# Performance work log

Hardware: AMD Instinct MI355X
Metric: run time of the kernel (lower is better)

Reference implementation:

```python
import jax, jax.numpy as jnp
import numpy as np

EPS = 1e-5  # torch F.layer_norm default

def _layer_norm(x):
    mu = jnp.mean(x, axis=-1, keepdims=True)
    var = jnp.mean((x - mu) ** 2, axis=-1, keepdims=True)
    return (x - mu) * jax.lax.rsqrt(var + EPS)

def setup_inputs() -> dict:
    key = jax.random.key(0)
    k1, k2, k3, k4 = jax.random.split(key, 4)
    B, T, d, n = 4, 32, 256, 1024
    return {
        "x_seq": jax.random.normal(k1, (B, T, d), jnp.float32),
        "targets": jax.random.normal(k2, (B, T, d), jnp.float32),
        "E": jax.random.normal(k3, (d, n), jnp.float32) * 0.1,
        "Dy": jax.random.normal(k4, (n, d), jnp.float32) * 0.1,
    }

def reference(x_seq, targets, E, Dy):
    B, T, d = x_seq.shape
    n = E.shape[1]
    # Precompute per-step neuron activations (no cross-step dependency here)
    x_neurons = jax.nn.relu(_layer_norm(x_seq @ E))      # [B,T,n]
    tgt_neurons = jax.nn.relu(_layer_norm(targets @ E))  # [B,T,n]
    # update at step t uses targets[:, t+1]; last step does no update
    tgt_next = jnp.concatenate(
        [tgt_neurons[:, 1:], jnp.zeros_like(tgt_neurons[:, :1])], axis=1)
    upd_mask = jnp.arange(T) < (T - 1)  # [T]

    G0 = jnp.tile(0.01 * jnp.eye(n, dtype=x_seq.dtype)[None], (B, 1, 1))

    def step(G, inp):
        xn, tn, m = inp  # [B,n], [B,n], scalar bool
        p1 = jnp.einsum('bn,bnm->bm', xn, G)
        p2 = jnp.einsum('bn,bnm->bm', p1, G)
        p3 = jnp.einsum('bn,bnm->bm', p2, G)
        reasoning = jnp.maximum(p1, jnp.maximum(p2, p3))
        y = jax.nn.relu(reasoning @ Dy)  # [B,d]
        # rank-1 Hebbian max-update: G = max(G, 0.5 * xn tn^T)
        upd = 0.5 * xn[:, :, None] * tn[:, None, :]
        G_new = jnp.where(m, jnp.maximum(G, upd), G)
        return G_new, y

    xs = (jnp.swapaxes(x_neurons, 0, 1),  # [T,B,n]
          jnp.swapaxes(tgt_next, 0, 1),   # [T,B,n]
          upd_mask)                       # [T]
    _, ys = jax.lax.scan(step, G0, xs)    # ys: [T,B,d]
    return jnp.swapaxes(ys, 0, 1)         # [B,T,d]
```

## Files before the change

### kernel.cpp

```cpp
#include <hip/hip_runtime.h>

#define BB 4
#define TT 32
#define DD 256
#define NN 1024

#define XN_OFF   0
#define TN_OFF   131072
#define PB_OFF   262144
#define RB_OFF   524288
#define FLG_OFF  655360
#define FLG_WORDS 6144
#define WS_END   (FLG_OFF + FLG_WORDS)

__global__ __launch_bounds__(256) void precompute_kernel(
    const float* __restrict__ x_seq, const float* __restrict__ targets,
    const float* __restrict__ E, float* __restrict__ ws)
{
    __shared__ float xr[4][DD];
    __shared__ float redS[4][4], redSS[4][4];
    const int blk = blockIdx.x;
    const int bt0 = blk * 2, bt1 = bt0 + 1;
    const int tid = threadIdx.x;
    const int lane = tid & 63, w = tid >> 6;

    xr[0][tid] = x_seq[(size_t)bt0 * DD + tid];
    xr[1][tid] = x_seq[(size_t)bt1 * DD + tid];
    xr[2][tid] = targets[(size_t)bt0 * DD + tid];
    xr[3][tid] = targets[(size_t)bt1 * DD + tid];
    __syncthreads();

    const float4* E4 = (const float4*)E;
    float4 acc[4];
#pragma unroll
    for (int r = 0; r < 4; ++r) acc[r] = make_float4(0.f, 0.f, 0.f, 0.f);
#pragma unroll 4
    for (int k = 0; k < DD; ++k) {
        float4 e = E4[(size_t)k * (NN / 4) + tid];
#pragma unroll
        for (int r = 0; r < 4; ++r) {
            float xv = xr[r][k];
            acc[r].x += xv * e.x; acc[r].y += xv * e.y;
            acc[r].z += xv * e.z; acc[r].w += xv * e.w;
        }
    }
    float s[4], ss[4];
#pragma unroll
    for (int r = 0; r < 4; ++r) {
        s[r]  = acc[r].x + acc[r].y + acc[r].z + acc[r].w;
        ss[r] = acc[r].x*acc[r].x + acc[r].y*acc[r].y + acc[r].z*acc[r].z + acc[r].w*acc[r].w;
    }
#pragma unroll
    for (int d = 1; d < 64; d <<= 1) {
#pragma unroll
        for (int r = 0; r < 4; ++r) {
            s[r]  += __shfl_xor(s[r], d, 64);
            ss[r] += __shfl_xor(ss[r], d, 64);
        }
    }
    if (lane == 0) {
#pragma unroll
        for (int r = 0; r < 4; ++r) { redS[w][r] = s[r]; redSS[w][r] = ss[r]; }
    }
    __syncthreads();
#pragma unroll
    for (int r = 0; r < 4; ++r) {
        s[r]  = redS[0][r] + redS[1][r] + redS[2][r] + redS[3][r];
        ss[r] = redSS[0][r] + redSS[1][r] + redSS[2][r] + redSS[3][r];
    }
#pragma unroll
    for (int r = 0; r < 4; ++r) {
        const float mu  = s[r] * (1.0f / NN);
        const float var = ss[r] * (1.0f / NN) - mu * mu;
        const float inv = rsqrtf(var + 1e-5f);
        float4 o;
        o.x = fmaxf(0.f, (acc[r].x - mu) * inv);
        o.y = fmaxf(0.f, (acc[r].y - mu) * inv);
        o.z = fmaxf(0.f, (acc[r].z - mu) * inv);
        o.w = fmaxf(0.f, (acc[r].w - mu) * inv);
        const int bt = (r & 1) ? bt1 : bt0;
        float* dst = nullptr;
        if (r < 2) dst = ws + XN_OFF + (size_t)bt * NN;
        else if ((bt & 31) > 0) dst = ws + TN_OFF + (size_t)(bt - 1) * NN;
        if (dst) ((float4*)dst)[tid] = o;
    }
}

__device__ __forceinline__ float ald(const float* p) {
    return __hip_atomic_load(p, __ATOMIC_RELAXED, __HIP_MEMORY_SCOPE_AGENT);
}
__device__ __forceinline__ unsigned long long ald64(const unsigned long long* p) {
    return __hip_atomic_load(p, __ATOMIC_RELAXED, __HIP_MEMORY_SCOPE_AGENT);
}
__device__ __forceinline__ void ast(float* p, float v) {
    __hip_atomic_store(p, v, __ATOMIC_RELAXED, __HIP_MEMORY_SCOPE_AGENT);
}
__device__ __forceinline__ unsigned aldu_rlx(const unsigned* p) {
    return __hip_atomic_load(p, __ATOMIC_RELAXED, __HIP_MEMORY_SCOPE_AGENT);
}

__global__ __launch_bounds__(512, 2) void mega_kernel(
    const float* __restrict__ Dy, float* __restrict__ out, float* __restrict__ ws)
{
    __shared__ float sh[6144];
    const int blk = blockIdx.x;
    const int tid = threadIdx.x;

    float* pb     = ws + PB_OFF;
    float* rb     = ws + RB_OFF;
    unsigned* flg = (unsigned*)(ws + FLG_OFF);

    if (blk < 192) {
        const int stage = blk >> 6;
        const int b     = (blk >> 4) & 3;
        const int wg    = blk & 15;
        const int lane  = tid & 63;
        const int w     = tid >> 6;
        const int colbase = wg * 64 + w * 8;
        const int row0    = lane * 16;
        const float* xn = ws + XN_OFF + (size_t)b * TT * NN;
        const float* tn = ws + TN_OFF + (size_t)b * TT * NN;
        unsigned* myflag = flg + ((size_t)(stage * 4 + b) * 16 + wg) * 32;
        const unsigned* inflags =
            (stage > 0) ? flg + ((size_t)((stage - 1) * 4 + b) * 16) * 32 : (const unsigned*)0;
        unsigned seen = 0;

        float G[16][8];
#pragma unroll
        for (int i = 0; i < 16; ++i)
#pragma unroll
            for (int c = 0; c < 8; ++c)
                G[i][c] = (row0 + i == colbase + c) ? 0.01f : 0.0f;

#pragma unroll 1
        for (int t = 0; t < TT; ++t) {
            const int bt = b * TT + t;
            float* p1 = pb + (size_t)bt * 2 * NN;
            float* p2 = p1 + NN;

            float in[16], x[16];
            float v1own = 0.f;
            if (stage == 0) {
                const float4* xp = (const float4*)(xn + (size_t)t * NN + row0);
                float4 q0 = xp[0], q1 = xp[1], q2 = xp[2], q3 = xp[3];
                in[0]=q0.x; in[1]=q0.y; in[2]=q0.z; in[3]=q0.w;
                in[4]=q1.x; in[5]=q1.y; in[6]=q1.z; in[7]=q1.w;
                in[8]=q2.x; in[9]=q2.y; in[10]=q2.z; in[11]=q2.w;
                in[12]=q3.x; in[13]=q3.y; in[14]=q3.z; in[15]=q3.w;
#pragma unroll
                for (int j = 0; j < 16; ++j) x[j] = in[j];
            } else {
                const unsigned tgt = (unsigned)(t + 1);
                if (tid < 64) {
                    if (seen < tgt) {
                        const unsigned* p = inflags + (size_t)(tid & 15) * 32;
                        int g = 0;
                        for (;;) {
                            unsigned v = aldu_rlx(p);
                            if (v > seen) seen = v;
                            if (__all(seen >= tgt)) break;
                            __builtin_amdgcn_s_sleep(1);
                            if (++g > (1 << 22)) break;
                        }
                    }
                }
                __syncthreads();
                asm volatile("" ::: "memory");
                if (stage == 2) v1own = ald(p1 + colbase + (lane & 7));
                const float* src = (stage == 1) ? p1 : p2;
                union { unsigned long long u; float f[2]; } cv;
                cv.u = ald64((const unsigned long long*)src + tid);
                const int e0 = 2 * tid;
                sh[e0 + (e0 >> 4)]     = cv.f[0];
                sh[e0 + 1 + (e0 >> 4)] = cv.f[1];
                __syncthreads();
#pragma unroll
                for (int j = 0; j < 16; ++j) in[j] = sh[lane * 17 + j];
            }

            float acc[8] = {0.f,0.f,0.f,0.f,0.f,0.f,0.f,0.f};
#pragma unroll
            for (int i = 0; i < 16; ++i)
#pragma unroll
                for (int c = 0; c < 8; ++c) acc[c] += in[i] * G[i][c];

            float t4[8];
#pragma unroll
            for (int c = 0; c < 8; ++c) t4[c] = __shfl_xor(acc[c], 4, 64);
            const bool k2 = (lane & 4) != 0;
            float s4[4];
#pragma unroll
            for (int k = 0; k < 4; ++k) s4[k] = k2 ? (acc[4+k] + t4[4+k]) : (acc[k] + t4[k]);
            float t2[4];
#pragma unroll
            for (int k = 0; k < 4; ++k) t2[k] = __shfl_xor(s4[k], 2, 64);
            const bool k1 = (lane & 2) != 0;
            float s2[2];
#pragma unroll
            for (int k = 0; k < 2; ++k) s2[k] = k1 ? (s4[2+k] + t2[2+k]) : (s4[k] + t2[k]);
            float t1[2];
#pragma unroll
            for (int k = 0; k < 2; ++k) t1[k] = __shfl_xor(s2[k], 1, 64);
            float v = (lane & 1) ? (s2[1] + t1[1]) : (s2[0] + t1[0]);
            v += __shfl_xor(v, 8, 64);
            v += __shfl_xor(v, 16, 64);
            v += __shfl_xor(v, 32, 64);

            if (stage == 0) {
                if (lane < 8) ast(p1 + colbase + lane, v);
            } else if (stage == 1) {
                if (lane < 8) ast(p2 + colbase + lane, v);
            } else {
                const int c = colbase + (lane & 7);
                const float v2own = sh[c + (c >> 4)];
                float r = fmaxf(v, fmaxf(v1own, v2own));
                if (lane < 8) ast(rb + (size_t)bt * NN + colbase + lane, r);
            }
            __syncthreads();
            if (tid == 0)
                __hip_atomic_store(myflag, (unsigned)(t + 1),
                                   __ATOMIC_RELEASE, __HIP_MEMORY_SCOPE_AGENT);

            if (t < TT - 1) {
                if (stage != 0) {
                    const float4* xp = (const float4*)(xn + (size_t)t * NN + row0);
                    float4 q0 = xp[0], q1 = xp[1], q2 = xp[2], q3 = xp[3];
                    x[0]=q0.x; x[1]=q0.y; x[2]=q0.z; x[3]=q0.w;
                    x[4]=q1.x; x[5]=q1.y; x[6]=q1.z; x[7]=q1.w;
                    x[8]=q2.x; x[9]=q2.y; x[10]=q2.z; x[11]=q2.w;
                    x[12]=q3.x; x[13]=q3.y; x[14]=q3.z; x[15]=q3.w;
                }
                const float4 ta = *(const float4*)(tn + (size_t)t * NN + colbase);
                const float4 tb = *(const float4*)(tn + (size_t)t * NN + colbase + 4);
                const float tv[8] = {0.5f*ta.x, 0.5f*ta.y, 0.5f*ta.z, 0.5f*ta.w,
                                     0.5f*tb.x, 0.5f*tb.y, 0.5f*tb.z, 0.5f*tb.w};
#pragma unroll
                for (int c = 0; c < 8; ++c)
#pragma unroll
                    for (int i = 0; i < 16; ++i)
                        G[i][c] = fmaxf(G[i][c], x[i] * tv[c]);
            }
        }
    } else {
        const int k   = blk - 192;
        const int b   = k >> 3;
        const int t0  = (k & 7) * 4;
        const int bt0 = b * TT + t0;
        if (tid < 64) {
            const unsigned* p = flg + ((size_t)(2 * 4 + b) * 16 + (tid & 15)) * 32;
            const unsigned tgt = (unsigned)(t0 + 4);
            int g = 0;
            for (;;) {
                unsigned v = aldu_rlx(p);
                if (__all(v >= tgt)) break;
                __builtin_amdgcn_s_sleep(1);
                if (++g > (1 << 22)) break;
            }
        }
        __syncthreads();
        asm volatile("" ::: "memory");
#pragma unroll
        for (int j = 0; j < 4; ++j) {
            const float* r = rb + (size_t)(bt0 + j) * NN;
            sh[tid * 4 + j]         = ald(r + tid);
            sh[(tid + 512) * 4 + j] = ald(r + tid + 512);
        }
        __syncthreads();
        const int d = tid & 255, h = tid >> 8;
        float acc[4] = {0.f, 0.f, 0.f, 0.f};
        const int n0 = h * 512;
#pragma unroll 8
        for (int n = n0; n < n0 + 512; ++n) {
            const float dv = Dy[(size_t)n * DD + d];
            const float4 rv = *(const float4*)&sh[n * 4];
            acc[0] += rv.x * dv; acc[1] += rv.y * dv;
            acc[2] += rv.z * dv; acc[3] += rv.w * dv;
        }
#pragma unroll
        for (int j = 0; j < 4; ++j) sh[4096 + (h * 4 + j) * 256 + d] = acc[j];
        __syncthreads();
        if (tid < 256) {
#pragma unroll
            for (int j = 0; j < 4; ++j)
                out[(size_t)(bt0 + j) * DD + tid] =
                    fmaxf(0.f, sh[4096 + j * 256 + tid] + sh[4096 + (4 + j) * 256 + tid]);
        }
    }
}

extern "C" void kernel_launch(void* const* d_in, const int* in_sizes, int n_in,
                              void* d_out, int out_size, void* d_ws, size_t ws_size,
                              hipStream_t stream) {
    const float* x_seq   = (const float*)d_in[0];
    const float* targets = (const float*)d_in[1];
    const float* E       = (const float*)d_in[2];
    const float* Dy      = (const float*)d_in[3];
    float* out = (float*)d_out;
    float* ws  = (float*)d_ws;

    hipMemsetAsync(ws + FLG_OFF, 0, (size_t)FLG_WORDS * sizeof(unsigned), stream);

    precompute_kernel<<<BB * TT / 2, 256, 0, stream>>>(x_seq, targets, E, ws);
    mega_kernel<<<224, 512, 0, stream>>>(Dy, out, ws);
}
```

Baseline: 242.2 us.

## Process two timesteps per flag handshake in pipelined stage blocks

Each stage block now handles timesteps t and t+1 per loop iteration. It waits on the upstream flag once for both, loads both input vectors together, and publishes a single flag after both products. This halves the number of cross-block spin-wait handshakes and barriers, but it makes downstream stages wait for two steps before they start, so pipeline fill latency grows. Launch bounds drop to one block per SM to allow more registers for the doubled state.

```diff
diff --git a/kernel.cpp b/kernel.cpp
--- a/kernel.cpp
+++ b/kernel.cpp
@@ -99,7 +99,7 @@
     return __hip_atomic_load(p, __ATOMIC_RELAXED, __HIP_MEMORY_SCOPE_AGENT);
 }
 
-__global__ __launch_bounds__(512, 2) void mega_kernel(
+__global__ __launch_bounds__(512, 1) void mega_kernel(
     const float* __restrict__ Dy, float* __restrict__ out, float* __restrict__ ws)
 {
     __shared__ float sh[6144];
@@ -133,24 +133,31 @@
                 G[i][c] = (row0 + i == colbase + c) ? 0.01f : 0.0f;
 
 #pragma unroll 1
-        for (int t = 0; t < TT; ++t) {
+        for (int t = 0; t < TT; t += 2) {
             const int bt = b * TT + t;
-            float* p1 = pb + (size_t)bt * 2 * NN;
-            float* p2 = p1 + NN;
-
-            float in[16], x[16];
-            float v1own = 0.f;
+            float* p1t = pb + (size_t)bt * 2 * NN;
+            float* p2t = p1t + NN;
+            float* p1u = p2t + NN;
+            float* p2u = p1u + NN;
+
+            float in_t[16], in_u[16];
+            float v1own_t = 0.f, v1own_u = 0.f;
+
             if (stage == 0) {
                 const float4* xp = (const float4*)(xn + (size_t)t * NN + row0);
+                const float4* xq = (const float4*)(xn + (size_t)(t + 1) * NN + row0);
                 float4 q0 = xp[0], q1 = xp[1], q2 = xp[2], q3 = xp[3];
-                in[0]=q0.x; in[1]=q0.y; in[2]=q0.z; in[3]=q0.w;
-                in[4]=q1.x; in[5]=q1.y; in[6]=q1.z; in[7]=q1.w;
-                in[8]=q2.x; in[9]=q2.y; in[10]=q2.z; in[11]=q2.w;
-                in[12]=q3.x; in[13]=q3.y; in[14]=q3.z; in[15]=q3.w;
-#pragma unroll
-                for (int j = 0; j < 16; ++j) x[j] = in[j];
+                float4 r0 = xq[0], r1 = xq[1], r2 = xq[2], r3 = xq[3];
+                in_t[0]=q0.x; in_t[1]=q0.y; in_t[2]=q0.z; in_t[3]=q0.w;
+                in_t[4]=q1.x; in_t[5]=q1.y; in_t[6]=q1.z; in_t[7]=q1.w;
+                in_t[8]=q2.x; in_t[9]=q2.y; in_t[10]=q2.z; in_t[11]=q2.w;
+                in_t[12]=q3.x; in_t[13]=q3.y; in_t[14]=q3.z; in_t[15]=q3.w;
+                in_u[0]=r0.x; in_u[1]=r0.y; in_u[2]=r0.z; in_u[3]=r0.w;
+                in_u[4]=r1.x; in_u[5]=r1.y; in_u[6]=r1.z; in_u[7]=r1.w;
+                in_u[8]=r2.x; in_u[9]=r2.y; in_u[10]=r2.z; in_u[11]=r2.w;
+                in_u[12]=r3.x; in_u[13]=r3.y; in_u[14]=r3.z; in_u[15]=r3.w;
             } else {
-                const unsigned tgt = (unsigned)(t + 1);
+                const unsigned tgt = (unsigned)(t + 2);
                 if (tid < 64) {
                     if (seen < tgt) {
                         const unsigned* p = inflags + (size_t)(tid & 15) * 32;
@@ -166,63 +173,74 @@
                 }
                 __syncthreads();
                 asm volatile("" ::: "memory");
-                if (stage == 2) v1own = ald(p1 + colbase + (lane & 7));
-                const float* src = (stage == 1) ? p1 : p2;
-                union { unsigned long long u; float f[2]; } cv;
-                cv.u = ald64((const unsigned long long*)src + tid);
+                if (stage == 2) {
+                    v1own_t = ald(p1t + colbase + (lane & 7));
+                    v1own_u = ald(p1u + colbase + (lane & 7));
+                }
+                const float* st = (stage == 1) ? p1t : p2t;
+                const float* su = (stage == 1) ? p1u : p2u;
+                union { unsigned long long u; float f[2]; } ct, cu;
+                ct.u = ald64((const unsigned long long*)st + tid);
+                cu.u = ald64((const unsigned long long*)su + tid);
                 const int e0 = 2 * tid;
-                sh[e0 + (e0 >> 4)]     = cv.f[0];
-                sh[e0 + 1 + (e0 >> 4)] = cv.f[1];
+                sh[e0 + (e0 >> 4)]            = ct.f[0];
+                sh[e0 + 1 + (e0 >> 4)]        = ct.f[1];
+                sh[1152 + e0 + (e0 >> 4)]     = cu.f[0];
+                sh[1152 + e0 + 1 + (e0 >> 4)] = cu.f[1];
                 __syncthreads();
 #pragma unroll
-                for (int j = 0; j < 16; ++j) in[j] = sh[lane * 17 + j];
-            }
-
-            float acc[8] = {0.f,0.f,0.f,0.f,0.f,0.f,0.f,0.f};
-#pragma unroll
-            for (int i = 0; i < 16; ++i)
-#pragma unroll
-                for (int c = 0; c < 8; ++c) acc[c] += in[i] * G[i][c];
-
-            float t4[8];
-#pragma unroll
-            for (int c = 0; c < 8; ++c) t4[c] = __shfl_xor(acc[c], 4, 64);
-            const bool k2 = (lane & 4) != 0;
-            float s4[4];
-#pragma unroll
-            for (int k = 0; k < 4; ++k) s4[k] = k2 ? (acc[4+k] + t4[4+k]) : (acc[k] + t4[k]);
-            float t2[4];
-#pragma unroll
-            for (int k = 0; k < 4; ++k) t2[k] = __shfl_xor(s4[k], 2, 64);
-            const bool k1 = (lane & 2) != 0;
-            float s2[2];
-#pragma unroll
-            for (int k = 0; k < 2; ++k) s2[k] = k1 ? (s4[2+k] + t2[2+k]) : (s4[k] + t2[k]);
-            float t1[2];
-#pragma unroll
-            for (int k = 0; k < 2; ++k) t1[k] = __shfl_xor(s2[k], 1, 64);
-            float v = (lane & 1) ? (s2[1] + t1[1]) : (s2[0] + t1[0]);
-            v += __shfl_xor(v, 8, 64);
-            v += __shfl_xor(v, 16, 64);
-            v += __shfl_xor(v, 32, 64);
-
-            if (stage == 0) {
-                if (lane < 8) ast(p1 + colbase + lane, v);
-            } else if (stage == 1) {
-                if (lane < 8) ast(p2 + colbase + lane, v);
-            } else {
-                const int c = colbase + (lane & 7);
-                const float v2own = sh[c + (c >> 4)];
-                float r = fmaxf(v, fmaxf(v1own, v2own));
-                if (lane < 8) ast(rb + (size_t)bt * NN + colbase + lane, r);
-            }
-            __syncthreads();
-            if (tid == 0)
-                __hip_atomic_store(myflag, (unsigned)(t + 1),
-                                   __ATOMIC_RELEASE, __HIP_MEMORY_SCOPE_AGENT);
-
-            if (t < TT - 1) {
-                if (stage != 0) {
+                for (int j = 0; j < 16; ++j) {
+                    in_t[j] = sh[lane * 17 + j];
+                    in_u[j] = sh[1152 + lane * 17 + j];
+                }
+            }
+
+            {
+                float acc[8] = {0.f,0.f,0.f,0.f,0.f,0.f,0.f,0.f};
+#pragma unroll
+                for (int i = 0; i < 16; ++i)
+#pragma unroll
+                    for (int c = 0; c < 8; ++c) acc[c] += in_t[i] * G[i][c];
+                float t4[8];
+#pragma unroll
+                for (int c = 0; c < 8; ++c) t4[c] = __shfl_xor(acc[c], 4, 64);
+                const bool k2 = (lane & 4) != 0;
+                float s4[4];
+#pragma unroll
+                for (int k = 0; k < 4; ++k) s4[k] = k2 ? (acc[4+k] + t4[4+k]) : (acc[k] + t4[k]);
+                float t2[4];
+#pragma unroll
+                for (int k = 0; k < 4; ++k) t2[k] = __shfl_xor(s4[k], 2, 64);
+                const bool k1 = (lane & 2) != 0;
+                float s2[2];
+#pragma unroll
+                for (int k = 0; k < 2; ++k) s2[k] = k1 ? (s4[2+k] + t2[2+k]) : (s4[k] + t2[k]);
+                float t1[2];
+#pragma unroll
+                for (int k = 0; k < 2; ++k) t1[k] = __shfl_xor(s2[k], 1, 64);
+                float v = (lane & 1) ? (s2[1] + t1[1]) : (s2[0] + t1[0]);
+                v += __shfl_xor(v, 8, 64);
+                v += __shfl_xor(v, 16, 64);
+                v += __shfl_xor(v, 32, 64);
+
+                if (stage == 0) {
+                    if (lane < 8) ast(p1t + colbase + lane, v);
+                } else if (stage == 1) {
+                    if (lane < 8) ast(p2t + colbase + lane, v);
+                } else {
+                    const int c = colbase + (lane & 7);
+                    const float v2own = sh[c + (c >> 4)];
+                    float r = fmaxf(v, fmaxf(v1own_t, v2own));
+                    if (lane < 8) ast(rb + (size_t)bt * NN + colbase + lane, r);
+                }
+            }
+
+            {
+                float x[16];
+                if (stage == 0) {
+#pragma unroll
+                    for (int j = 0; j < 16; ++j) x[j] = in_t[j];
+                } else {
                     const float4* xp = (const float4*)(xn + (size_t)t * NN + row0);
                     float4 q0 = xp[0], q1 = xp[1], q2 = xp[2], q3 = xp[3];
                     x[0]=q0.x; x[1]=q0.y; x[2]=q0.z; x[3]=q0.w;
@@ -232,6 +250,75 @@
                 }
                 const float4 ta = *(const float4*)(tn + (size_t)t * NN + colbase);
                 const float4 tb = *(const float4*)(tn + (size_t)t * NN + colbase + 4);
+                const float tv[8] = {0.5f*ta.x, 0.5f*ta.y, 0.5f*ta.z, 0.5f*ta.w,
+                                     0.5f*tb.x, 0.5f*tb.y, 0.5f*tb.z, 0.5f*tb.w};
+#pragma unroll
+                for (int c = 0; c < 8; ++c)
+#pragma unroll
+                    for (int i = 0; i < 16; ++i)
+                        G[i][c] = fmaxf(G[i][c], x[i] * tv[c]);
+            }
+
+            {
+                float acc[8] = {0.f,0.f,0.f,0.f,0.f,0.f,0.f,0.f};
+#pragma unroll
+                for (int i = 0; i < 16; ++i)
+#pragma unroll
+                    for (int c = 0; c < 8; ++c) acc[c] += in_u[i] * G[i][c];
+                float t4[8];
+#pragma unroll
+                for (int c = 0; c < 8; ++c) t4[c] = __shfl_xor(acc[c], 4, 64);
+                const bool k2 = (lane & 4) != 0;
+                float s4[4];
+#pragma unroll
+                for (int k = 0; k < 4; ++k) s4[k] = k2 ? (acc[4+k] + t4[4+k]) : (acc[k] + t4[k]);
+                float t2[4];
+#pragma unroll
+                for (int k = 0; k < 4; ++k) t2[k] = __shfl_xor(s4[k], 2, 64);
+                const bool k1 = (lane & 2) != 0;
+                float s2[2];
+#pragma unroll
+                for (int k = 0; k < 2; ++k) s2[k] = k1 ? (s4[2+k] + t2[2+k]) : (s4[k] + t2[k]);
+                float t1[2];
+#pragma unroll
+                for (int k = 0; k < 2; ++k) t1[k] = __shfl_xor(s2[k], 1, 64);
+                float v = (lane & 1) ? (s2[1] + t1[1]) : (s2[0] + t1[0]);
+                v += __shfl_xor(v, 8, 64);
+                v += __shfl_xor(v, 16, 64);
+                v += __shfl_xor(v, 32, 64);
+
+                if (stage == 0) {
+                    if (lane < 8) ast(p1u + colbase + lane, v);
+                } else if (stage == 1) {
+                    if (lane < 8) ast(p2u + colbase + lane, v);
+                } else {
+                    const int c = colbase + (lane & 7);
+                    const float v2own = sh[1152 + c + (c >> 4)];
+                    float r = fmaxf(v, fmaxf(v1own_u, v2own));
+                    if (lane < 8) ast(rb + (size_t)(bt + 1) * NN + colbase + lane, r);
+                }
+            }
+
+            __syncthreads();
+            if (tid == 0)
+                __hip_atomic_store(myflag, (unsigned)(t + 2),
+                                   __ATOMIC_RELEASE, __HIP_MEMORY_SCOPE_AGENT);
+
+            if (t + 1 < TT - 1) {
+                float x[16];
+                if (stage == 0) {
+#pragma unroll
+                    for (int j = 0; j < 16; ++j) x[j] = in_u[j];
+                } else {
+                    const float4* xp = (const float4*)(xn + (size_t)(t + 1) * NN + row0);
+                    float4 q0 = xp[0], q1 = xp[1], q2 = xp[2], q3 = xp[3];
+                    x[0]=q0.x; x[1]=q0.y; x[2]=q0.z; x[3]=q0.w;
+                    x[4]=q1.x; x[5]=q1.y; x[6]=q1.z; x[7]=q1.w;
+                    x[8]=q2.x; x[9]=q2.y; x[10]=q2.z; x[11]=q2.w;
+                    x[12]=q3.x; x[13]=q3.y; x[14]=q3.z; x[15]=q3.w;
+                }
+                const float4 ta = *(const float4*)(tn + (size_t)(t + 1) * NN + colbase);
+                const float4 tb = *(const float4*)(tn + (size_t)(t + 1) * NN + colbase + 4);
                 const float tv[8] = {0.5f*ta.x, 0.5f*ta.y, 0.5f*ta.z, 0.5f*ta.w,
                                      0.5f*tb.x, 0.5f*tb.y, 0.5f*tb.z, 0.5f*tb.w};
 #pragma unroll
```

Result: faster. 213.6 us (-11.8%).

## Batch four timesteps per inter-stage flag handoff in the pipelined scan kernel

Applied to the files above, without the earlier changes.

The three-stage G-propagation pipeline now processes timesteps in chunks of four, with one flag wait and one flag publish per chunk. Previously it synchronised across blocks on every timestep. The consumer stages load four timesteps' worth of p1/p2 vectors into shared memory at once, and the Hebbian max-updates for the first three steps run inside the chunk. This is meant to cut the number of cross-block spin-wait round trips, at the cost of a coarser pipeline fill latency between stages. Launch bounds drop to one block per CU to give the compiler more registers for the unrolled chunk.

```diff
diff --git a/kernel.cpp b/kernel.cpp
--- a/kernel.cpp
+++ b/kernel.cpp
@@ -99,7 +99,7 @@
     return __hip_atomic_load(p, __ATOMIC_RELAXED, __HIP_MEMORY_SCOPE_AGENT);
 }
 
-__global__ __launch_bounds__(512, 2) void mega_kernel(
+__global__ __launch_bounds__(512, 1) void mega_kernel(
     const float* __restrict__ Dy, float* __restrict__ out, float* __restrict__ ws)
 {
     __shared__ float sh[6144];
@@ -133,24 +133,14 @@
                 G[i][c] = (row0 + i == colbase + c) ? 0.01f : 0.0f;
 
 #pragma unroll 1
-        for (int t = 0; t < TT; ++t) {
+        for (int t = 0; t < TT; t += 4) {
             const int bt = b * TT + t;
-            float* p1 = pb + (size_t)bt * 2 * NN;
-            float* p2 = p1 + NN;
-
-            float in[16], x[16];
-            float v1own = 0.f;
-            if (stage == 0) {
-                const float4* xp = (const float4*)(xn + (size_t)t * NN + row0);
-                float4 q0 = xp[0], q1 = xp[1], q2 = xp[2], q3 = xp[3];
-                in[0]=q0.x; in[1]=q0.y; in[2]=q0.z; in[3]=q0.w;
-                in[4]=q1.x; in[5]=q1.y; in[6]=q1.z; in[7]=q1.w;
-                in[8]=q2.x; in[9]=q2.y; in[10]=q2.z; in[11]=q2.w;
-                in[12]=q3.x; in[13]=q3.y; in[14]=q3.z; in[15]=q3.w;
-#pragma unroll
-                for (int j = 0; j < 16; ++j) x[j] = in[j];
-            } else {
-                const unsigned tgt = (unsigned)(t + 1);
+            float* pbase = pb + (size_t)bt * 2 * NN;
+
+            float v1own[4] = {0.f, 0.f, 0.f, 0.f};
+
+            if (stage != 0) {
+                const unsigned tgt = (unsigned)(t + 4);
                 if (tid < 64) {
                     if (seen < tgt) {
                         const unsigned* p = inflags + (size_t)(tid & 15) * 32;
@@ -166,72 +156,132 @@
                 }
                 __syncthreads();
                 asm volatile("" ::: "memory");
-                if (stage == 2) v1own = ald(p1 + colbase + (lane & 7));
-                const float* src = (stage == 1) ? p1 : p2;
-                union { unsigned long long u; float f[2]; } cv;
-                cv.u = ald64((const unsigned long long*)src + tid);
+                if (stage == 2) {
+#pragma unroll
+                    for (int j = 0; j < 4; ++j)
+                        v1own[j] = ald(pbase + (size_t)(2 * j) * NN + colbase + (lane & 7));
+                }
+                union { unsigned long long u; float f[2]; } cv[4];
+#pragma unroll
+                for (int j = 0; j < 4; ++j) {
+                    const float* src = pbase + (size_t)(2 * j) * NN + ((stage == 1) ? 0 : NN);
+                    cv[j].u = ald64((const unsigned long long*)src + tid);
+                }
                 const int e0 = 2 * tid;
-                sh[e0 + (e0 >> 4)]     = cv.f[0];
-                sh[e0 + 1 + (e0 >> 4)] = cv.f[1];
+#pragma unroll
+                for (int j = 0; j < 4; ++j) {
+                    sh[j * 1152 + e0 + (e0 >> 4)]     = cv[j].f[0];
+                    sh[j * 1152 + e0 + 1 + (e0 >> 4)] = cv[j].f[1];
+                }
                 __syncthreads();
-#pragma unroll
-                for (int j = 0; j < 16; ++j) in[j] = sh[lane * 17 + j];
             }
 
-            float acc[8] = {0.f,0.f,0.f,0.f,0.f,0.f,0.f,0.f};
-#pragma unroll
-            for (int i = 0; i < 16; ++i)
-#pragma unroll
-                for (int c = 0; c < 8; ++c) acc[c] += in[i] * G[i][c];
-
-            float t4[8];
-#pragma unroll
-            for (int c = 0; c < 8; ++c) t4[c] = __shfl_xor(acc[c], 4, 64);
-            const bool k2 = (lane & 4) != 0;
-            float s4[4];
-#pragma unroll
-            for (int k = 0; k < 4; ++k) s4[k] = k2 ? (acc[4+k] + t4[4+k]) : (acc[k] + t4[k]);
-            float t2[4];
-#pragma unroll
-            for (int k = 0; k < 4; ++k) t2[k] = __shfl_xor(s4[k], 2, 64);
-            const bool k1 = (lane & 2) != 0;
-            float s2[2];
-#pragma unroll
-            for (int k = 0; k < 2; ++k) s2[k] = k1 ? (s4[2+k] + t2[2+k]) : (s4[k] + t2[k]);
-            float t1[2];
-#pragma unroll
-            for (int k = 0; k < 2; ++k) t1[k] = __shfl_xor(s2[k], 1, 64);
-            float v = (lane & 1) ? (s2[1] + t1[1]) : (s2[0] + t1[0]);
-            v += __shfl_xor(v, 8, 64);
-            v += __shfl_xor(v, 16, 64);
-            v += __shfl_xor(v, 32, 64);
-
-            if (stage == 0) {
-                if (lane < 8) ast(p1 + colbase + lane, v);
-            } else if (stage == 1) {
-                if (lane < 8) ast(p2 + colbase + lane, v);
-            } else {
-                const int c = colbase + (lane & 7);
-                const float v2own = sh[c + (c >> 4)];
-                float r = fmaxf(v, fmaxf(v1own, v2own));
-                if (lane < 8) ast(rb + (size_t)bt * NN + colbase + lane, r);
+            float xsave[16];
+#pragma unroll
+            for (int j = 0; j < 4; ++j) {
+                const int tj = t + j;
+                float in[16];
+                if (stage == 0) {
+                    const float4* xp = (const float4*)(xn + (size_t)tj * NN + row0);
+                    float4 q0 = xp[0], q1 = xp[1], q2 = xp[2], q3 = xp[3];
+                    in[0]=q0.x; in[1]=q0.y; in[2]=q0.z; in[3]=q0.w;
+                    in[4]=q1.x; in[5]=q1.y; in[6]=q1.z; in[7]=q1.w;
+                    in[8]=q2.x; in[9]=q2.y; in[10]=q2.z; in[11]=q2.w;
+                    in[12]=q3.x; in[13]=q3.y; in[14]=q3.z; in[15]=q3.w;
+                    if (j == 3) {
+#pragma unroll
+                        for (int k = 0; k < 16; ++k) xsave[k] = in[k];
+                    }
+                } else {
+#pragma unroll
+                    for (int k = 0; k < 16; ++k) in[k] = sh[j * 1152 + lane * 17 + k];
+                }
+
+                float acc[8] = {0.f,0.f,0.f,0.f,0.f,0.f,0.f,0.f};
+#pragma unroll
+                for (int i = 0; i < 16; ++i)
+#pragma unroll
+                    for (int c = 0; c < 8; ++c) acc[c] += in[i] * G[i][c];
+
+                float t4[8];
+#pragma unroll
+                for (int c = 0; c < 8; ++c) t4[c] = __shfl_xor(acc[c], 4, 64);
+                const bool k2 = (lane & 4) != 0;
+                float s4[4];
+#pragma unroll
+                for (int k = 0; k < 4; ++k) s4[k] = k2 ? (acc[4+k] + t4[4+k]) : (acc[k] + t4[k]);
+                float t2[4];
+#pragma unroll
+                for (int k = 0; k < 4; ++k) t2[k] = __shfl_xor(s4[k], 2, 64);
+                const bool k1 = (lane & 2) != 0;
+                float s2[2];
+#pragma unroll
+                for (int k = 0; k < 2; ++k) s2[k] = k1 ? (s4[2+k] + t2[2+k]) : (s4[k] + t2[k]);
+                float t1[2];
+#pragma unroll
+                for (int k = 0; k < 2; ++k) t1[k] = __shfl_xor(s2[k], 1, 64);
+                float v = (lane & 1) ? (s2[1] + t1[1]) : (s2[0] + t1[0]);
+                v += __shfl_xor(v, 8, 64);
+                v += __shfl_xor(v, 16, 64);
+                v += __shfl_xor(v, 32, 64);
+
+                if (stage == 0) {
+                    if (lane < 8) ast(pbase + (size_t)(2 * j) * NN + colbase + lane, v);
+                } else if (stage == 1) {
+                    if (lane < 8) ast(pbase + (size_t)(2 * j) * NN + NN + colbase + lane, v);
+                } else {
+                    const int c = colbase + (lane & 7);
+                    const float v2own = sh[j * 1152 + c + (c >> 4)];
+                    float r = fmaxf(v, fmaxf(v1own[j], v2own));
+                    if (lane < 8) ast(rb + (size_t)(bt + j) * NN + colbase + lane, r);
+                }
+
+                if (j < 3) {
+                    float x[16];
+                    if (stage == 0) {
+#pragma unroll
+                        for (int k = 0; k < 16; ++k) x[k] = in[k];
+                    } else {
+                        const float4* xp = (const float4*)(xn + (size_t)tj * NN + row0);
+                        float4 q0 = xp[0], q1 = xp[1], q2 = xp[2], q3 = xp[3];
+                        x[0]=q0.x; x[1]=q0.y; x[2]=q0.z; x[3]=q0.w;
+                        x[4]=q1.x; x[5]=q1.y; x[6]=q1.z; x[7]=q1.w;
+                        x[8]=q2.x; x[9]=q2.y; x[10]=q2.z; x[11]=q2.w;
+                        x[12]=q3.x; x[13]=q3.y; x[14]=q3.z; x[15]=q3.w;
+                    }
+                    const float4 ta = *(const float4*)(tn + (size_t)tj * NN + colbase);
+                    const float4 tb = *(const float4*)(tn + (size_t)tj * NN + colbase + 4);
+                    const float tv[8] = {0.5f*ta.x, 0.5f*ta.y, 0.5f*ta.z, 0.5f*ta.w,
+                                         0.5f*tb.x, 0.5f*tb.y, 0.5f*tb.z, 0.5f*tb.w};
+#pragma unroll
+                    for (int c = 0; c < 8; ++c)
+#pragma unroll
+                        for (int i = 0; i < 16; ++i)
+                            G[i][c] = fmaxf(G[i][c], x[i] * tv[c]);
+                }
             }
+
             __syncthreads();
             if (tid == 0)
-                __hip_atomic_store(myflag, (unsigned)(t + 1),
+                __hip_atomic_store(myflag, (unsigned)(t + 4),
                                    __ATOMIC_RELEASE, __HIP_MEMORY_SCOPE_AGENT);
 
-            if (t < TT - 1) {
-                if (stage != 0) {
-                    const float4* xp = (const float4*)(xn + (size_t)t * NN + row0);
+            if (t + 3 < TT - 1) {
+                const int tj = t + 3;
+                float x[16];
+                if (stage == 0) {
+#pragma unroll
+                    for (int k = 0; k < 16; ++k) x[k] = xsave[k];
+                } else {
+                    const float4* xp = (const float4*)(xn + (size_t)tj * NN + row0);
                     float4 q0 = xp[0], q1 = xp[1], q2 = xp[2], q3 = xp[3];
                     x[0]=q0.x; x[1]=q0.y; x[2]=q0.z; x[3]=q0.w;
                     x[4]=q1.x; x[5]=q1.y; x[6]=q1.z; x[7]=q1.w;
                     x[8]=q2.x; x[9]=q2.y; x[10]=q2.z; x[11]=q2.w;
                     x[12]=q3.x; x[13]=q3.y; x[14]=q3.z; x[15]=q3.w;
                 }
-                const float4 ta = *(const float4*)(tn + (size_t)t * NN + colbase);
-                const float4 tb = *(const float4*)(tn + (size_t)t * NN + colbase + 4);
+                const float4 ta = *(const float4*)(tn + (size_t)tj * NN + colbase);
+                const float4 tb = *(const float4*)(tn + (size_t)tj * NN + colbase + 4);
                 const float tv[8] = {0.5f*ta.x, 0.5f*ta.y, 0.5f*ta.z, 0.5f*ta.w,
                                      0.5f*tb.x, 0.5f*tb.y, 0.5f*tb.z, 0.5f*tb.w};
 #pragma unroll
```

Result: slower. 247.4 us (+2.1%).
